# Optimization experiments

Hardware: AMD Instinct MI355X
Metric: run time of the kernel (lower is better)

## Reference

```python
import jax, jax.numpy as jnp
import numpy as np
import math

N_HEADS = 16
FACTOR = 5

def setup_inputs() -> dict:
    key = jax.random.key(0)
    ks = jax.random.split(key, 9)
    B, T, D = 4, 2048, 1024
    w = lambda k: jax.random.normal(k, (D, D), dtype=jnp.float32) * 0.02
    return {
        "x": jax.random.normal(ks[0], (B, T, D), dtype=jnp.float32),
        "Wq": w(ks[1]), "bq": jnp.zeros((D,), jnp.float32),
        "Wk": w(ks[2]), "bk": jnp.zeros((D,), jnp.float32),
        "Wv": w(ks[3]), "bv": jnp.zeros((D,), jnp.float32),
        "Wo": w(ks[4]), "bo": jnp.zeros((D,), jnp.float32),
    }

def reference(x, Wq, bq, Wk, bk, Wv, bv, Wo, bo):
    B, T, D = x.shape
    H = N_HEADS
    hd = D // H
    scale = hd ** (-0.5)

    def proj(W, b):
        # [B,T,D] -> [B,H,T,hd]
        return (x @ W + b).reshape(B, T, H, hd).transpose(0, 2, 1, 3)

    q = proj(Wq, bq)
    k = proj(Wk, bk)
    v = proj(Wv, bv)

    # top-u query selection by L1 norm per (b,h)
    u = min(int(FACTOR * math.log(T)), T)
    q_norm = jnp.sum(jnp.abs(q), axis=-1)          # [B,H,T]
    _, idx = jax.lax.top_k(q_norm, u)              # [B,H,u]

    # gather selected queries; compute only the u selected score rows
    q_sel = jnp.take_along_axis(q, idx[..., None], axis=2)  # [B,H,u,hd]
    sel_scores = jnp.einsum('bhud,bhtd->bhut', q_sel, k) * scale  # [B,H,u,T]

    # causal mask for selected rows: key pos j attends iff j <= query pos
    causal = jnp.arange(T)[None, None, None, :] <= idx[..., None]  # [B,H,u,T]
    sel_scores = jnp.where(causal, sel_scores, -jnp.inf)

    attn = jax.nn.softmax(sel_scores, axis=-1)     # dropout omitted (eval)
    sel_out = jnp.einsum('bhut,bhtd->bhud', attn, v)  # [B,H,u,hd]

    # scatter selected rows back into zeros (non-selected rows stay 0)
    bi = jnp.arange(B)[:, None, None]
    hi = jnp.arange(H)[None, :, None]
    attn_out = jnp.zeros((B, H, T, hd), x.dtype).at[bi, hi, idx].set(sel_out)

    out = attn_out.transpose(0, 2, 1, 3).reshape(B, T, D)
    return out @ Wo + bo
```

## Files before the change

### kernel.cpp

```cpp
#include <hip/hip_runtime.h>
#include <hip/hip_bf16.h>
#include <math.h>

#define B_  4
#define T_  2048
#define D_  1024
#define H_  16
#define HD_ 64
#define U_  38
#define M_  (B_*T_)
#define NCW_ 32

typedef __attribute__((ext_vector_type(8))) short bf16x8;
typedef __attribute__((ext_vector_type(4))) float f32x4;

__device__ __forceinline__ short f2b(float f) {
    __hip_bfloat16 b = __float2bfloat16(f);
    return *(short*)&b;
}
__device__ __forceinline__ float b2f(short s) {
    __hip_bfloat16 b = *(__hip_bfloat16*)&s;
    return __bfloat162float(b);
}
__device__ __forceinline__ unsigned pack2(float lo, float hi) {
    unsigned a = (unsigned short)f2b(lo);
    unsigned b = ((unsigned)(unsigned short)f2b(hi)) << 16;
    return a | b;
}

__device__ __forceinline__ void gload16(const void* g, void* l) {
    __builtin_amdgcn_global_load_lds(
        (const __attribute__((address_space(1))) unsigned int*)g,
        (__attribute__((address_space(3))) unsigned int*)l,
        16, 0, 0);
}

__global__ __launch_bounds__(256) void convx_kernel(
    const float* __restrict__ x, short* __restrict__ xh, short* __restrict__ xl)
{
    const size_t i = ((size_t)blockIdx.x * 256 + threadIdx.x) * 4;
    float4 v = *(const float4*)(x + i);
    short4 h, l;
    h.x = f2b(v.x); l.x = f2b(v.x - b2f(h.x));
    h.y = f2b(v.y); l.y = f2b(v.y - b2f(h.y));
    h.z = f2b(v.z); l.z = f2b(v.z - b2f(h.z));
    h.w = f2b(v.w); l.w = f2b(v.w - b2f(h.w));
    *(short4*)(xh + i) = h;
    *(short4*)(xl + i) = l;
}

__global__ __launch_bounds__(256) void convw_kernel(
    const float* __restrict__ Wq, const float* __restrict__ Wk, const float* __restrict__ Wv,
    short* __restrict__ wq2, short* __restrict__ wkvt)
{
    __shared__ float tile[32][33];
    const int which = blockIdx.z;
    const float* W = which == 0 ? Wq : (which == 1 ? Wk : Wv);
    const int k0 = blockIdx.y * 32, n0 = blockIdx.x * 32;
    const int tx = threadIdx.x & 31, ty = threadIdx.x >> 5;
    #pragma unroll
    for (int r = ty; r < 32; r += 8)
        tile[r][tx] = W[(size_t)(k0 + r) * D_ + n0 + tx];
    __syncthreads();
    #pragma unroll
    for (int r = ty; r < 32; r += 8) {
        float v = tile[tx][r];
        size_t o = (size_t)(n0 + r) * D_ + k0 + tx;
        if (which == 0) {
            short h = f2b(v);
            wq2[o] = h;
            wq2[o + 1048576] = f2b(v - b2f(h));
        } else {
            wkvt[(size_t)(which - 1) * D_ * D_ + o] = f2b(v);
        }
    }
}

__global__ __launch_bounds__(256) void gemm_fused(
    const short* __restrict__ xh, const short* __restrict__ xl,
    const short* __restrict__ wq2, const short* __restrict__ wkvt,
    const float* __restrict__ bq, const float* __restrict__ bk,
    const float* __restrict__ bv,
    float* __restrict__ qnorm, short* __restrict__ qbuf,
    short* __restrict__ kb, short* __restrict__ vt)
{
    __shared__ short As[128 * 64];
    __shared__ short Bs[128 * 64];
    const int bid = blockIdx.x;
    const bool isQ = bid < 512;
    const int tid = threadIdx.x, wid = tid >> 6, lane = tid & 63;
    const int l15 = lane & 15, gr = lane >> 4;
    const int lb = isQ ? bid : bid - 512;
    const int m0 = (lb & 63) * 128;
    const int n0 = (lb >> 6) * 128;
    const int wr = (wid >> 1) * 64, wc = (wid & 1) * 64;

    f32x4 acc[4][4];
    #pragma unroll
    for (int i = 0; i < 4; ++i)
        #pragma unroll
        for (int j = 0; j < 4; ++j)
            acc[i][j] = (f32x4){0.f, 0.f, 0.f, 0.f};

    const int KT = isQ ? 48 : 16;
    for (int kt = 0; kt < KT; ++kt) {
        const short* Asrc;
        const short* Bsrc;
        int ka;
        if (isQ) {
            const int sec = kt >> 4;
            Asrc = (sec == 1) ? xl : xh;
            Bsrc = wq2 + (sec == 2 ? 1048576 : 0);
            ka = (kt & 15) * 64;
        } else {
            Asrc = xh; Bsrc = wkvt; ka = kt * 64;
        }
        #pragma unroll
        for (int i = 0; i < 4; ++i) {
            const int e = tid + i * 256;
            const int row = e >> 3;
            const int soff = ((e & 7) ^ (row & 7)) * 8;
            gload16(Asrc + (size_t)(m0 + row) * D_ + ka + soff,
                    (char*)As + i * 4096 + wid * 1024);
            gload16(Bsrc + (size_t)(n0 + row) * D_ + ka + soff,
                    (char*)Bs + i * 4096 + wid * 1024);
        }
        __syncthreads();
        #pragma unroll
        for (int ks = 0; ks < 2; ++ks) {
            bf16x8 a[4], b[4];
            #pragma unroll
            for (int i = 0; i < 4; ++i)
                a[i] = *(bf16x8*)((char*)As + (wr + i * 16 + l15) * 128
                                   + (((ks << 2) | gr) ^ (l15 & 7)) * 16);
            #pragma unroll
            for (int j = 0; j < 4; ++j)
                b[j] = *(bf16x8*)((char*)Bs + (wc + j * 16 + l15) * 128
                                   + (((ks << 2) | gr) ^ (l15 & 7)) * 16);
            #pragma unroll
            for (int i = 0; i < 4; ++i)
                #pragma unroll
                for (int j = 0; j < 4; ++j)
                    acc[i][j] = __builtin_amdgcn_mfma_f32_16x16x32_bf16(a[i], b[j], acc[i][j], 0, 0, 0);
        }
        __syncthreads();
    }

    if (isQ) {
        const int h = (n0 + wc) >> 6;
        #pragma unroll
        for (int i = 0; i < 4; ++i)
            #pragma unroll
            for (int r = 0; r < 4; ++r) {
                int row = m0 + wr + i * 16 + gr * 4 + r;
                float s = 0.f;
                #pragma unroll
                for (int j = 0; j < 4; ++j) {
                    int col = n0 + wc + j * 16 + l15;
                    float val = acc[i][j][r] + bq[col];
                    qbuf[(size_t)row * D_ + col] = f2b(val);
                    s += fabsf(val);
                }
                s += __shfl_xor(s, 1);
                s += __shfl_xor(s, 2);
                s += __shfl_xor(s, 4);
                s += __shfl_xor(s, 8);
                if (l15 == 0) {
                    int b = row >> 11, t = row & (T_ - 1);
                    qnorm[((size_t)b * H_ + h) * T_ + t] = s;
                }
            }
    } else {
        #pragma unroll
        for (int i = 0; i < 4; ++i)
            #pragma unroll
            for (int j = 0; j < 4; ++j) {
                const int col = n0 + wc + j * 16 + l15;
                const int rowb = m0 + wr + i * 16 + gr * 4;
                const int bb = rowb >> 11, t0 = rowb & (T_ - 1);
                if (col < D_) {
                    const int hh = col >> 6, dd = col & 63;
                    const float bias = bk[col];
                    #pragma unroll
                    for (int r = 0; r < 4; ++r)
                        kb[(((size_t)bb * H_ + hh) * T_ + t0 + r) * HD_ + dd] =
                            f2b(acc[i][j][r] + bias);
                } else {
                    const int cc2 = col - D_;
                    const int hh = cc2 >> 6, dd = cc2 & 63;
                    const float bias = bv[cc2];
                    short4 pk;
                    pk.x = f2b(acc[i][j][0] + bias);
                    pk.y = f2b(acc[i][j][1] + bias);
                    pk.z = f2b(acc[i][j][2] + bias);
                    pk.w = f2b(acc[i][j][3] + bias);
                    *(short4*)(vt + (((size_t)bb * H_ + hh) * HD_ + dd) * T_ + t0) = pk;
                }
            }
    }
}

__global__ __launch_bounds__(64) void topk_kernel(
    const float* __restrict__ qnorm, int* __restrict__ idxout)
{
    const int g = blockIdx.x;
    const int lane = threadIdx.x;
    float v[32];
    const float* src = qnorm + (size_t)g * T_ + lane * 32;
    #pragma unroll
    for (int i = 0; i < 32; i += 4) {
        float4 t = *(const float4*)(src + i);
        v[i] = t.x; v[i + 1] = t.y; v[i + 2] = t.z; v[i + 3] = t.w;
    }
    unsigned removed = 0;
    float lm; int li;
    #pragma unroll
    for (int it = 0; it < U_ + 1; ++it) {
        lm = -3e38f; li = 0;
        #pragma unroll
        for (int i = 0; i < 32; ++i) {
            bool ok = !((removed >> i) & 1u) && v[i] > lm;
            lm = ok ? v[i] : lm;
            li = ok ? i : li;
        }
        if (it == U_) break;
        float bm = lm; int bi = lane * 32 + li;
        #pragma unroll
        for (int off = 32; off; off >>= 1) {
            float om = __shfl_xor(bm, off);
            int   oi = __shfl_xor(bi, off);
            if (om > bm || (om == bm && oi < bi)) { bm = om; bi = oi; }
        }
        if (lane == 0) idxout[g * U_ + it] = bi;
        if ((bi >> 5) == lane) removed |= 1u << (bi & 31);
    }
}

__global__ __launch_bounds__(256) void attn_part(
    const short* __restrict__ qbuf, const short* __restrict__ kb,
    const short* __restrict__ vt, const int* __restrict__ idxb,
    float* __restrict__ pm, float* __restrict__ pl, float* __restrict__ po)
{
    __shared__ short qs[48 * 72];
    __shared__ short pls[4][48 * 72];
    __shared__ int   sidx[48];
    const int bid = blockIdx.x;
    const int g = bid & 63;
    const int c = bid >> 6;
    const int b = g >> 4, h = g & 15;
    const int tid = threadIdx.x, wid = tid >> 6, lane = tid & 63;
    const int l15 = lane & 15, gr = lane >> 4;
    const int cw = c * 4 + wid;
    const int j0w = cw * 64;

    if (tid < 48) sidx[tid] = (tid < U_) ? idxb[g * U_ + tid] : 0;
    __syncthreads();
    for (int e = tid; e < 48 * 16; e += 256) {
        int u = e >> 4, d4 = e & 15;
        short4 v = make_short4(0, 0, 0, 0);
        if (u < U_)
            v = *(const short4*)(qbuf + ((size_t)b * T_ + sidx[u]) * D_ + h * HD_ + d4 * 4);
        *(short4*)&qs[u * 72 + d4 * 4] = v;
    }
    __syncthreads();

    int su[3];
    #pragma unroll
    for (int uf = 0; uf < 3; ++uf) su[uf] = sidx[uf * 16 + l15];

    f32x4 accs[3][4];
    #pragma unroll
    for (int uf = 0; uf < 3; ++uf)
        #pragma unroll
        for (int jf = 0; jf < 4; ++jf)
            accs[uf][jf] = (f32x4){0.f, 0.f, 0.f, 0.f};

    bf16x8 ka[4][2], qb[3][2];
    #pragma unroll
    for (int jf = 0; jf < 4; ++jf)
        #pragma unroll
        for (int ks = 0; ks < 2; ++ks)
            ka[jf][ks] = *(const bf16x8*)(kb + ((size_t)g * T_ + j0w + jf * 16 + l15) * HD_ + ks * 32 + gr * 8);
    #pragma unroll
    for (int uf = 0; uf < 3; ++uf)
        #pragma unroll
        for (int ks = 0; ks < 2; ++ks)
            qb[uf][ks] = *(bf16x8*)&qs[(uf * 16 + l15) * 72 + ks * 32 + gr * 8];

    #pragma unroll
    for (int uf = 0; uf < 3; ++uf)
        #pragma unroll
        for (int jf = 0; jf < 4; ++jf) {
            accs[uf][jf] = __builtin_amdgcn_mfma_f32_16x16x32_bf16(ka[jf][0], qb[uf][0], accs[uf][jf], 0, 0, 0);
            accs[uf][jf] = __builtin_amdgcn_mfma_f32_16x16x32_bf16(ka[jf][1], qb[uf][1], accs[uf][jf], 0, 0, 0);
        }

    #pragma unroll
    for (int uf = 0; uf < 3; ++uf) {
        float mm = -3e38f;
        #pragma unroll
        for (int jf = 0; jf < 4; ++jf)
            #pragma unroll
            for (int r = 0; r < 4; ++r) {
                int j = j0w + jf * 16 + gr * 4 + r;
                float s = accs[uf][jf][r] * 0.125f;
                s = (j <= su[uf]) ? s : -1e30f;
                accs[uf][jf][r] = s;
                mm = fmaxf(mm, s);
            }
        mm = fmaxf(mm, __shfl_xor(mm, 16));
        mm = fmaxf(mm, __shfl_xor(mm, 32));
        float ll = 0.f;
        #pragma unroll
        for (int jf = 0; jf < 4; ++jf)
            #pragma unroll
            for (int r = 0; r < 4; ++r) {
                float e = __expf(accs[uf][jf][r] - mm);
                accs[uf][jf][r] = e;
                ll += e;
            }
        ll += __shfl_xor(ll, 16);
        ll += __shfl_xor(ll, 32);
        if (gr == 0) {
            int u = uf * 16 + l15;
            if (u < U_) {
                pm[((size_t)g * NCW_ + cw) * U_ + u] = mm;
                pl[((size_t)g * NCW_ + cw) * U_ + u] = ll;
            }
        }
    }

    short* pw = &pls[wid][0];
    #pragma unroll
    for (int uf = 0; uf < 3; ++uf)
        #pragma unroll
        for (int jf = 0; jf < 4; ++jf) {
            uint2 wv;
            wv.x = pack2(accs[uf][jf][0], accs[uf][jf][1]);
            wv.y = pack2(accs[uf][jf][2], accs[uf][jf][3]);
            *(uint2*)&pw[(uf * 16 + l15) * 72 + jf * 16 + gr * 4] = wv;
        }

    bf16x8 va[4][2], pb[3][2];
    #pragma unroll
    for (int df = 0; df < 4; ++df)
        #pragma unroll
        for (int ks = 0; ks < 2; ++ks)
            va[df][ks] = *(const bf16x8*)(vt + ((size_t)g * HD_ + df * 16 + l15) * T_ + j0w + ks * 32 + gr * 8);
    #pragma unroll
    for (int uf = 0; uf < 3; ++uf)
        #pragma unroll
        for (int ks = 0; ks < 2; ++ks)
            pb[uf][ks] = *(bf16x8*)&pw[(uf * 16 + l15) * 72 + ks * 32 + gr * 8];

    f32x4 acco[4][3];
    #pragma unroll
    for (int df = 0; df < 4; ++df)
        #pragma unroll
        for (int uf = 0; uf < 3; ++uf)
            acco[df][uf] = (f32x4){0.f, 0.f, 0.f, 0.f};
    #pragma unroll
    for (int df = 0; df < 4; ++df)
        #pragma unroll
        for (int uf = 0; uf < 3; ++uf) {
            acco[df][uf] = __builtin_amdgcn_mfma_f32_16x16x32_bf16(va[df][0], pb[uf][0], acco[df][uf], 0, 0, 0);
            acco[df][uf] = __builtin_amdgcn_mfma_f32_16x16x32_bf16(va[df][1], pb[uf][1], acco[df][uf], 0, 0, 0);
        }

    #pragma unroll
    for (int df = 0; df < 4; ++df)
        #pragma unroll
        for (int uf = 0; uf < 3; ++uf) {
            int u = uf * 16 + l15;
            if (u < U_) {
                float4 o;
                o.x = acco[df][uf][0]; o.y = acco[df][uf][1];
                o.z = acco[df][uf][2]; o.w = acco[df][uf][3];
                *(float4*)(po + (((size_t)g * NCW_ + cw) * U_ + u) * HD_ + df * 16 + gr * 4) = o;
            }
        }
}

__global__ __launch_bounds__(256) void attn_combine(
    const float* __restrict__ pm, const float* __restrict__ pl,
    const float* __restrict__ po, float* __restrict__ selo)
{
    const int g = blockIdx.x;
    const int u = blockIdx.y * 4 + (threadIdx.x >> 6);
    const int d = threadIdx.x & 63;
    if (u >= U_) return;

    const float* pmg = pm + (size_t)g * NCW_ * U_ + u;
    const float* plg = pl + (size_t)g * NCW_ * U_ + u;

    float mc[NCW_];
    #pragma unroll
    for (int c = 0; c < NCW_; ++c) mc[c] = pmg[(size_t)c * U_];
    float m = -3e38f;
    #pragma unroll
    for (int c = 0; c < NCW_; ++c) m = fmaxf(m, mc[c]);

    float w[NCW_];
    #pragma unroll
    for (int c = 0; c < NCW_; ++c) w[c] = __expf(mc[c] - m);

    float l = 0.f;
    #pragma unroll
    for (int c = 0; c < NCW_; ++c) l += plg[(size_t)c * U_] * w[c];

    float o = 0.f;
    #pragma unroll
    for (int c = 0; c < NCW_; ++c)
        o += po[(((size_t)g * NCW_ + c) * U_ + u) * HD_ + d] * w[c];

    selo[((size_t)g * U_ + u) * HD_ + d] = o / l;
}

__global__ __launch_bounds__(256) void fill_kernel(
    const float* __restrict__ bo, float* __restrict__ out)
{
    const size_t i = (size_t)blockIdx.x * 256 + threadIdx.x;
    float4 bv = *(const float4*)(bo + ((i & 255) << 2));
    *(float4*)(out + i * 4) = bv;
}

__global__ __launch_bounds__(256) void oproj_kernel(
    const float* __restrict__ selo, const int* __restrict__ idxb,
    const float* __restrict__ Wo, float* __restrict__ out)
{
    __shared__ float sel[64];
    const int blk = blockIdx.x;
    const int h = (blk / U_) % H_;
    const int b = blk / (U_ * H_);
    const int t = idxb[blk];
    const int tid = threadIdx.x;
    if (tid < 64) sel[tid] = selo[(size_t)blk * HD_ + tid];
    __syncthreads();
    float* orow = out + ((size_t)b * T_ + t) * D_;
    #pragma unroll
    for (int rep = 0; rep < 4; ++rep) {
        int n = tid + rep * 256;
        float c = 0.f;
        #pragma unroll 8
        for (int dd = 0; dd < 64; ++dd)
            c += sel[dd] * Wo[(size_t)(h * HD_ + dd) * D_ + n];
        atomicAdd(orow + n, c);
    }
}

extern "C" void kernel_launch(void* const* d_in, const int* in_sizes, int n_in,
                              void* d_out, int out_size, void* d_ws, size_t ws_size,
                              hipStream_t stream)
{
    const float* x  = (const float*)d_in[0];
    const float* Wq = (const float*)d_in[1];
    const float* bq = (const float*)d_in[2];
    const float* Wk = (const float*)d_in[3];
    const float* bk = (const float*)d_in[4];
    const float* Wv = (const float*)d_in[5];
    const float* bv = (const float*)d_in[6];
    const float* Wo = (const float*)d_in[7];
    const float* bo = (const float*)d_in[8];
    float* out = (float*)d_out;

    char* ws = (char*)d_ws;
    short* xh    = (short*)(ws);
    short* xl    = (short*)(ws + 16777216);
    short* wq2   = (short*)(ws + 33554432);
    short* wkvt  = (short*)(ws + 37748736);
    short* kb    = (short*)(ws + 41943040);
    short* vt    = (short*)(ws + 58720256);
    float* qnorm = (float*)(ws + 75497472);
    int*   idxb  = (int*)  (ws + 76021760);
    float* selo  = (float*)(ws + 76038144);
    short* qbuf  = (short*)(ws + 76660736);
    float* po    = (float*)(ws);
    float* pm    = (float*)(ws + 19922944);
    float* pl    = (float*)(ws + 20234240);

    convx_kernel<<<M_ * D_ / 1024, 256, 0, stream>>>(x, xh, xl);
    convw_kernel<<<dim3(32, 32, 3), 256, 0, stream>>>(Wq, Wk, Wv, wq2, wkvt);
    gemm_fused<<<1536, 256, 0, stream>>>(xh, xl, wq2, wkvt, bq, bk, bv,
                                         qnorm, qbuf, kb, vt);
    topk_kernel<<<B_ * H_, 64, 0, stream>>>(qnorm, idxb);
    attn_part<<<64 * 8, 256, 0, stream>>>(qbuf, kb, vt, idxb, pm, pl, po);
    attn_combine<<<dim3(B_ * H_, (U_ + 3) / 4), 256, 0, stream>>>(pm, pl, po, selo);
    fill_kernel<<<(M_ * D_ / 4) / 256, 256, 0, stream>>>(bo, out);
    oproj_kernel<<<B_ * H_ * U_, 256, 0, stream>>>(selo, idxb, Wo, out);
}
```

Before: 208.9 us.

## Select top-k candidates from low-precision Q norms, recompute precise Q only for candidates

The Q projection in the main GEMM now uses only the bf16-high parts of x and Wq (16 k-steps instead of 48) and no longer writes the full Q buffer; it only produces approximate L1 norms. A radix-style binary search picks the 144 highest-norm candidates per (batch, head). These are recomputed at split-bf16 precision in a small MFMA kernel, and a final top-38 selection runs on the precise norms. This removes two thirds of the Q-projection work and the full Q store, at the risk of missing a true top-k query whose approximate norm ranks outside the candidate set.

New measurement: 222.9 us. +6.7%, slower.

```diff
diff --git a/kernel.cpp b/kernel.cpp
--- a/kernel.cpp
+++ b/kernel.cpp
@@ -10,6 +10,7 @@
 #define U_  38
 #define M_  (B_*T_)
 #define NCW_ 32
+#define NC_ 144
 
 typedef __attribute__((ext_vector_type(8))) short bf16x8;
 typedef __attribute__((ext_vector_type(4))) float f32x4;
@@ -77,12 +78,11 @@
 }
 
 __global__ __launch_bounds__(256) void gemm_fused(
-    const short* __restrict__ xh, const short* __restrict__ xl,
-    const short* __restrict__ wq2, const short* __restrict__ wkvt,
+    const short* __restrict__ xh, const short* __restrict__ wq2,
+    const short* __restrict__ wkvt,
     const float* __restrict__ bq, const float* __restrict__ bk,
     const float* __restrict__ bv,
-    float* __restrict__ qnorm, short* __restrict__ qbuf,
-    short* __restrict__ kb, short* __restrict__ vt)
+    float* __restrict__ qnorm, short* __restrict__ kb, short* __restrict__ vt)
 {
     __shared__ short As[128 * 64];
     __shared__ short Bs[128 * 64];
@@ -102,19 +102,11 @@
         for (int j = 0; j < 4; ++j)
             acc[i][j] = (f32x4){0.f, 0.f, 0.f, 0.f};
 
-    const int KT = isQ ? 48 : 16;
-    for (int kt = 0; kt < KT; ++kt) {
-        const short* Asrc;
-        const short* Bsrc;
-        int ka;
-        if (isQ) {
-            const int sec = kt >> 4;
-            Asrc = (sec == 1) ? xl : xh;
-            Bsrc = wq2 + (sec == 2 ? 1048576 : 0);
-            ka = (kt & 15) * 64;
-        } else {
-            Asrc = xh; Bsrc = wkvt; ka = kt * 64;
-        }
+    const short* Asrc = xh;
+    const short* Bsrc = isQ ? wq2 : wkvt;
+
+    for (int kt = 0; kt < 16; ++kt) {
+        const int ka = kt * 64;
         #pragma unroll
         for (int i = 0; i < 4; ++i) {
             const int e = tid + i * 256;
@@ -157,9 +149,7 @@
                 #pragma unroll
                 for (int j = 0; j < 4; ++j) {
                     int col = n0 + wc + j * 16 + l15;
-                    float val = acc[i][j][r] + bq[col];
-                    qbuf[(size_t)row * D_ + col] = f2b(val);
-                    s += fabsf(val);
+                    s += fabsf(acc[i][j][r] + bq[col]);
                 }
                 s += __shfl_xor(s, 1);
                 s += __shfl_xor(s, 2);
@@ -200,45 +190,150 @@
     }
 }
 
-__global__ __launch_bounds__(64) void topk_kernel(
-    const float* __restrict__ qnorm, int* __restrict__ idxout)
+__global__ __launch_bounds__(64) void cand_kernel(
+    const float* __restrict__ qnorm, int* __restrict__ cand)
 {
     const int g = blockIdx.x;
     const int lane = threadIdx.x;
-    float v[32];
+    unsigned v[32];
     const float* src = qnorm + (size_t)g * T_ + lane * 32;
     #pragma unroll
     for (int i = 0; i < 32; i += 4) {
         float4 t = *(const float4*)(src + i);
-        v[i] = t.x; v[i + 1] = t.y; v[i + 2] = t.z; v[i + 3] = t.w;
-    }
-    unsigned removed = 0;
-    float lm; int li;
-    #pragma unroll
-    for (int it = 0; it < U_ + 1; ++it) {
-        lm = -3e38f; li = 0;
-        #pragma unroll
-        for (int i = 0; i < 32; ++i) {
-            bool ok = !((removed >> i) & 1u) && v[i] > lm;
-            lm = ok ? v[i] : lm;
-            li = ok ? i : li;
-        }
-        if (it == U_) break;
-        float bm = lm; int bi = lane * 32 + li;
-        #pragma unroll
+        v[i] = __float_as_uint(t.x); v[i + 1] = __float_as_uint(t.y);
+        v[i + 2] = __float_as_uint(t.z); v[i + 3] = __float_as_uint(t.w);
+    }
+    unsigned lo = 0, hi = 0x7F800000u;
+    while (lo < hi) {
+        unsigned mid = lo + ((hi - lo) >> 1);
+        int c = 0;
+        #pragma unroll
+        for (int i = 0; i < 32; ++i) c += (v[i] >= mid) ? 1 : 0;
+        #pragma unroll
+        for (int off = 1; off < 64; off <<= 1) c += __shfl_xor(c, off);
+        if (c <= NC_) hi = mid; else lo = mid + 1;
+    }
+    const unsigned tau = lo;
+    int myc = 0;
+    #pragma unroll
+    for (int i = 0; i < 32; ++i) myc += (v[i] >= tau) ? 1 : 0;
+    int inc = myc;
+    for (int off = 1; off < 64; off <<= 1) {
+        int n = __shfl_up(inc, off);
+        if (lane >= off) inc += n;
+    }
+    const int total = __shfl(inc, 63);
+    int pos = inc - myc;
+    #pragma unroll
+    for (int i = 0; i < 32; ++i)
+        if (v[i] >= tau) cand[g * NC_ + pos++] = lane * 32 + i;
+    for (int p = total + lane; p < NC_; p += 64)
+        cand[g * NC_ + p] = -1;
+}
+
+__global__ __launch_bounds__(64) void recheck_kernel(
+    const short* __restrict__ xh, const short* __restrict__ xl,
+    const short* __restrict__ wq2, const float* __restrict__ bq,
+    const int* __restrict__ cand,
+    float* __restrict__ cnorm, short* __restrict__ candq)
+{
+    const int blk = blockIdx.x;
+    const int g = blk / 9, rt = blk % 9;
+    const int b = g >> 4, h = g & 15;
+    const int lane = threadIdx.x, l15 = lane & 15, gr = lane >> 4;
+
+    const int aslot = rt * 16 + l15;
+    int at = cand[g * NC_ + aslot];
+    const size_t arow = ((size_t)b * T_ + (at < 0 ? 0 : at)) * D_;
+
+    f32x4 acc[4];
+    #pragma unroll
+    for (int j = 0; j < 4; ++j) acc[j] = (f32x4){0.f, 0.f, 0.f, 0.f};
+
+    const short* wqh = wq2;
+    const short* wql = wq2 + 1048576;
+    for (int kt = 0; kt < 32; ++kt) {
+        const int k0 = kt * 32 + gr * 8;
+        bf16x8 ah = *(const bf16x8*)(xh + arow + k0);
+        bf16x8 al = *(const bf16x8*)(xl + arow + k0);
+        #pragma unroll
+        for (int j = 0; j < 4; ++j) {
+            const size_t wrow = (size_t)(h * HD_ + j * 16 + l15) * D_ + k0;
+            bf16x8 bh = *(const bf16x8*)(wqh + wrow);
+            bf16x8 bl = *(const bf16x8*)(wql + wrow);
+            acc[j] = __builtin_amdgcn_mfma_f32_16x16x32_bf16(ah, bh, acc[j], 0, 0, 0);
+            acc[j] = __builtin_amdgcn_mfma_f32_16x16x32_bf16(ah, bl, acc[j], 0, 0, 0);
+            acc[j] = __builtin_amdgcn_mfma_f32_16x16x32_bf16(al, bh, acc[j], 0, 0, 0);
+        }
+    }
+
+    #pragma unroll
+    for (int r = 0; r < 4; ++r) {
+        const int slot = rt * 16 + gr * 4 + r;
+        float s = 0.f;
+        #pragma unroll
+        for (int j = 0; j < 4; ++j) {
+            const int col = j * 16 + l15;
+            float val = acc[j][r] + bq[h * HD_ + col];
+            candq[((size_t)g * NC_ + slot) * HD_ + col] = f2b(val);
+            s += fabsf(val);
+        }
+        s += __shfl_xor(s, 1);
+        s += __shfl_xor(s, 2);
+        s += __shfl_xor(s, 4);
+        s += __shfl_xor(s, 8);
+        if (l15 == 0) {
+            int ct = cand[g * NC_ + slot];
+            cnorm[g * NC_ + slot] = (ct < 0) ? -3e38f : s;
+        }
+    }
+}
+
+__global__ __launch_bounds__(64) void topk38_kernel(
+    const float* __restrict__ cnorm, const int* __restrict__ cand,
+    int* __restrict__ idxb, int* __restrict__ slotb)
+{
+    const int g = blockIdx.x;
+    const int lane = threadIdx.x;
+    float v[3]; int tt[3];
+    #pragma unroll
+    for (int i = 0; i < 3; ++i) {
+        int s = lane + 64 * i;
+        if (s < NC_) {
+            v[i] = cnorm[g * NC_ + s];
+            int c = cand[g * NC_ + s];
+            tt[i] = (c < 0) ? (1 << 30) : c;
+            if (c < 0) v[i] = -3e38f;
+        } else { v[i] = -3e38f; tt[i] = 1 << 30; }
+    }
+    for (int it = 0; it < U_; ++it) {
+        float bv = -3e38f; int bt = 1 << 30, bi = 0;
+        #pragma unroll
+        for (int i = 0; i < 3; ++i) {
+            bool better = (v[i] > bv) || (v[i] == bv && tt[i] < bt);
+            if (better) { bv = v[i]; bt = tt[i]; bi = i; }
+        }
+        int bs = lane + 64 * bi;
         for (int off = 32; off; off >>= 1) {
-            float om = __shfl_xor(bm, off);
-            int   oi = __shfl_xor(bi, off);
-            if (om > bm || (om == bm && oi < bi)) { bm = om; bi = oi; }
-        }
-        if (lane == 0) idxout[g * U_ + it] = bi;
-        if ((bi >> 5) == lane) removed |= 1u << (bi & 31);
+            float ov = __shfl_xor(bv, off);
+            int ot = __shfl_xor(bt, off);
+            int os = __shfl_xor(bs, off);
+            if (ov > bv || (ov == bv && ot < bt)) { bv = ov; bt = ot; bs = os; }
+        }
+        if (lane == 0) { idxb[g * U_ + it] = bt; slotb[g * 40 + it] = bs; }
+        if ((bs & 63) == lane) {
+            int wi = bs >> 6;
+            if (wi == 0) v[0] = -3e38f;
+            else if (wi == 1) v[1] = -3e38f;
+            else v[2] = -3e38f;
+        }
     }
 }
 
 __global__ __launch_bounds__(256) void attn_part(
-    const short* __restrict__ qbuf, const short* __restrict__ kb,
-    const short* __restrict__ vt, const int* __restrict__ idxb,
+    const short* __restrict__ candq, const int* __restrict__ slotb,
+    const short* __restrict__ kb, const short* __restrict__ vt,
+    const int* __restrict__ idxb,
     float* __restrict__ pm, float* __restrict__ pl, float* __restrict__ po)
 {
     __shared__ short qs[48 * 72];
@@ -247,7 +342,6 @@
     const int bid = blockIdx.x;
     const int g = bid & 63;
     const int c = bid >> 6;
-    const int b = g >> 4, h = g & 15;
     const int tid = threadIdx.x, wid = tid >> 6, lane = tid & 63;
     const int l15 = lane & 15, gr = lane >> 4;
     const int cw = c * 4 + wid;
@@ -258,8 +352,10 @@
     for (int e = tid; e < 48 * 16; e += 256) {
         int u = e >> 4, d4 = e & 15;
         short4 v = make_short4(0, 0, 0, 0);
-        if (u < U_)
-            v = *(const short4*)(qbuf + ((size_t)b * T_ + sidx[u]) * D_ + h * HD_ + d4 * 4);
+        if (u < U_) {
+            int slot = slotb[g * 40 + u];
+            v = *(const short4*)(candq + ((size_t)g * NC_ + slot) * HD_ + d4 * 4);
+        }
         *(short4*)&qs[u * 72 + d4 * 4] = v;
     }
     __syncthreads();
@@ -473,17 +569,21 @@
     float* qnorm = (float*)(ws + 75497472);
     int*   idxb  = (int*)  (ws + 76021760);
     float* selo  = (float*)(ws + 76038144);
-    short* qbuf  = (short*)(ws + 76660736);
+    int*   cand  = (int*)  (ws + 76660736);
+    float* cnorm = (float*)(ws + 76697600);
+    int*   slotb = (int*)  (ws + 76734464);
+    short* candq = (short*)(ws + 76750848);
     float* po    = (float*)(ws);
     float* pm    = (float*)(ws + 19922944);
     float* pl    = (float*)(ws + 20234240);
 
     convx_kernel<<<M_ * D_ / 1024, 256, 0, stream>>>(x, xh, xl);
     convw_kernel<<<dim3(32, 32, 3), 256, 0, stream>>>(Wq, Wk, Wv, wq2, wkvt);
-    gemm_fused<<<1536, 256, 0, stream>>>(xh, xl, wq2, wkvt, bq, bk, bv,
-                                         qnorm, qbuf, kb, vt);
-    topk_kernel<<<B_ * H_, 64, 0, stream>>>(qnorm, idxb);
-    attn_part<<<64 * 8, 256, 0, stream>>>(qbuf, kb, vt, idxb, pm, pl, po);
+    gemm_fused<<<1536, 256, 0, stream>>>(xh, wq2, wkvt, bq, bk, bv, qnorm, kb, vt);
+    cand_kernel<<<B_ * H_, 64, 0, stream>>>(qnorm, cand);
+    recheck_kernel<<<B_ * H_ * 9, 64, 0, stream>>>(xh, xl, wq2, bq, cand, cnorm, candq);
+    topk38_kernel<<<B_ * H_, 64, 0, stream>>>(cnorm, cand, idxb, slotb);
+    attn_part<<<64 * 8, 256, 0, stream>>>(candq, slotb, kb, vt, idxb, pm, pl, po);
     attn_combine<<<dim3(B_ * H_, (U_ + 3) / 4), 256, 0, stream>>>(pm, pl, po, selo);
     fill_kernel<<<(M_ * D_ / 4) / 256, 256, 0, stream>>>(bo, out);
     oproj_kernel<<<B_ * H_ * U_, 256, 0, stream>>>(selo, idxb, Wo, out);
```
